# Kernel tuning notes

Hardware: AMD Instinct MI355X
Metric: run time of the kernel (lower is better)

The kernel has to match this reference:

```python
import jax, jax.numpy as jnp
import numpy as np

N_NODES = 100000
N_EDGES = 1600000
IN_DIM = 128
HID_DIM = 128
OUT_DIM = 2


def sage_conv(x, src, dst, deg_inv, W_l, W_r, b):
    # mean-aggregate neighbor features: messages flow src -> dst
    agg = jax.ops.segment_sum(x[src], dst, num_segments=N_NODES)  # [N, d_in]
    agg = agg * deg_inv[:, None]
    # PyG SAGEConv: out = lin_l(aggr) + lin_r(x); bias only on lin_l
    return agg @ W_l + x @ W_r + b


def setup_inputs() -> dict:
    key = jax.random.key(0)
    ks = jax.random.split(key, 9)
    x = jax.random.normal(ks[0], (N_NODES, IN_DIM), dtype=jnp.float32)
    edge_index = jax.random.randint(ks[1], (2, N_EDGES), 0, N_NODES, dtype=jnp.int64)

    def glorot(k, shape):
        lim = float(np.sqrt(6.0 / (shape[0] + shape[1])))
        return jax.random.uniform(k, shape, jnp.float32, -lim, lim)

    return {
        "x": x,
        "edge_index": edge_index,
        "W1_l": glorot(ks[2], (IN_DIM, HID_DIM)),
        "W1_r": glorot(ks[3], (IN_DIM, HID_DIM)),
        "b1": jnp.zeros((HID_DIM,), jnp.float32),
        "W2_l": glorot(ks[4], (HID_DIM, HID_DIM)),
        "W2_r": glorot(ks[5], (HID_DIM, HID_DIM)),
        "b2": jnp.zeros((HID_DIM,), jnp.float32),
        "W3_l": glorot(ks[6], (HID_DIM, OUT_DIM)),
        "W3_r": glorot(ks[7], (HID_DIM, OUT_DIM)),
        "b3": jnp.zeros((OUT_DIM,), jnp.float32),
    }


def reference(x, edge_index, W1_l, W1_r, b1, W2_l, W2_r, b2, W3_l, W3_r, b3):
    src, dst = edge_index[0], edge_index[1]
    # mean-aggregation normalization: 1/in-degree (clamped to >=1)
    deg = jax.ops.segment_sum(jnp.ones((N_EDGES,), jnp.float32), dst, num_segments=N_NODES)
    deg_inv = 1.0 / jnp.maximum(deg, 1.0)

    h = sage_conv(x, src, dst, deg_inv, W1_l, W1_r, b1)
    h = jax.nn.relu(h)  # dropout is identity in eval mode
    h = sage_conv(h, src, dst, deg_inv, W2_l, W2_r, b2)
    h = jax.nn.relu(h)
    h = sage_conv(h, src, dst, deg_inv, W3_l, W3_r, b3)
    h = jax.nn.relu(h)
    return jax.nn.log_softmax(h, axis=1)
```

## Files before the change

kernel.cpp:

```cpp
#include <hip/hip_runtime.h>
#include <hip/hip_bf16.h>
#include <math.h>

#define DIM 128

typedef __attribute__((ext_vector_type(8))) short bf16x8;
typedef __attribute__((ext_vector_type(4))) float f32x4;

__device__ __forceinline__ ushort f2bf(float f) {
  unsigned u = __float_as_uint(f);
  return (ushort)((u + 0x7FFFu + ((u >> 16) & 1u)) >> 16);
}
__device__ __forceinline__ float bf2f(ushort h) {
  return __uint_as_float(((unsigned)h) << 16);
}

__global__ __launch_bounds__(256) void prep_kernel(
    const int* __restrict__ dst, unsigned* __restrict__ deg, unsigned* __restrict__ rank, int E,
    const float* __restrict__ x, ushort* __restrict__ xh, long total,
    const float* __restrict__ W1l, const float* __restrict__ W1r,
    const float* __restrict__ W2l, const float* __restrict__ W2r,
    ushort* __restrict__ tabs, int H, int C) {
  int bid = blockIdx.x;
  if (bid < H) {
    int gid = bid * 256 + threadIdx.x;
    if (gid < E) rank[gid] = atomicAdd(&deg[dst[gid]], 1u);
    return;
  }
  bid -= H;
  if (bid < C) {
    long i = ((long)bid * 256 + threadIdx.x) * 4;
    if (i >= total) return;
    float4 v = *(const float4*)(x + i);
    uint2 Hh;
    Hh.x = (unsigned)f2bf(v.x) | ((unsigned)f2bf(v.y) << 16);
    Hh.y = (unsigned)f2bf(v.z) | ((unsigned)f2bf(v.w) << 16);
    *(uint2*)(xh + i) = Hh;
    return;
  }
  bid -= C;
  int m = bid >> 6;
  const float* W = (m == 0) ? W1l : (m == 1) ? W1r : (m == 2) ? W2l : W2r;
  ushort* Ht = tabs + (size_t)m * 32768;
  ushort* Lt = Ht + 16384;
  int idx = (bid & 63) * 256 + threadIdx.x;
  int k = idx >> 7, n = idx & 127;
  float v = W[idx];
  ushort h = f2bf(v);
  Ht[n * DIM + k] = h;
  Lt[n * DIM + k] = f2bf(v - bf2f(h));
}

__global__ __launch_bounds__(256) void scan_block_kernel(const unsigned* __restrict__ deg,
                                                         unsigned* __restrict__ excl,
                                                         unsigned* __restrict__ partial,
                                                         float* __restrict__ dinv, int N) {
  __shared__ unsigned s[256];
  int i = blockIdx.x * 256 + threadIdx.x;
  unsigned v = (i < N) ? deg[i] : 0u;
  if (i < N) dinv[i] = 1.0f / fmaxf((float)v, 1.0f);
  s[threadIdx.x] = v;
  __syncthreads();
#pragma unroll
  for (int d = 1; d < 256; d <<= 1) {
    unsigned t = (threadIdx.x >= d) ? s[threadIdx.x - d] : 0u;
    __syncthreads();
    s[threadIdx.x] += t;
    __syncthreads();
  }
  if (i < N) excl[i] = s[threadIdx.x] - v;
  if (threadIdx.x == 255) partial[blockIdx.x] = s[255];
}

__global__ __launch_bounds__(256) void scan_partials_kernel(unsigned* __restrict__ partial, int B) {
  __shared__ unsigned s[256];
  __shared__ unsigned carry;
  if (threadIdx.x == 0) carry = 0u;
  __syncthreads();
  for (int base = 0; base < B; base += 256) {
    int i = base + threadIdx.x;
    unsigned v = (i < B) ? partial[i] : 0u;
    s[threadIdx.x] = v;
    __syncthreads();
#pragma unroll
    for (int d = 1; d < 256; d <<= 1) {
      unsigned t = (threadIdx.x >= d) ? s[threadIdx.x - d] : 0u;
      __syncthreads();
      s[threadIdx.x] += t;
      __syncthreads();
    }
    if (i < B) partial[i] = carry + s[threadIdx.x] - v;
    __syncthreads();
    if (threadIdx.x == 0) carry += s[255];
    __syncthreads();
  }
}

__global__ __launch_bounds__(256) void add_offsets_kernel(const unsigned* __restrict__ excl,
                                                          const unsigned* __restrict__ partial,
                                                          unsigned* __restrict__ off, int N, int E) {
  int i = blockIdx.x * 256 + threadIdx.x;
  if (i < N) off[i] = excl[i] + partial[i >> 8];
  if (i == N) off[N] = (unsigned)E;
}

__global__ __launch_bounds__(256) void csr_fill_kernel(const int* __restrict__ src,
                                                       const int* __restrict__ dst,
                                                       const unsigned* __restrict__ rank,
                                                       const unsigned* __restrict__ off,
                                                       int* __restrict__ csr_src, int E) {
  int e = blockIdx.x * 256 + threadIdx.x;
  if (e >= E) return;
  csr_src[off[dst[e]] + rank[e]] = src[e];
}

__global__ __launch_bounds__(256) void gather_wave_kernel(
    const ushort* __restrict__ featH, const int* __restrict__ csr_src,
    const unsigned* __restrict__ off, const float* __restrict__ dinv,
    ushort* __restrict__ aggH, int N) {
  const int node = (blockIdx.x * 256 + threadIdx.x) >> 6;
  if (node >= N) return;
  const int lane = threadIdx.x & 63;
  const int eslot = lane >> 4;
  const int col = lane & 15;
  const unsigned beg = off[node], end = off[node + 1];
  const ushort* fbase = featH + col * 8;

  float acc[8];
#pragma unroll
  for (int t = 0; t < 8; ++t) acc[t] = 0.f;

  auto accum = [&](int4 v) {
    unsigned w0 = (unsigned)v.x, w1 = (unsigned)v.y, w2 = (unsigned)v.z, w3 = (unsigned)v.w;
    acc[0] += __uint_as_float(w0 << 16);
    acc[1] += __uint_as_float(w0 & 0xFFFF0000u);
    acc[2] += __uint_as_float(w1 << 16);
    acc[3] += __uint_as_float(w1 & 0xFFFF0000u);
    acc[4] += __uint_as_float(w2 << 16);
    acc[5] += __uint_as_float(w2 & 0xFFFF0000u);
    acc[6] += __uint_as_float(w3 << 16);
    acc[7] += __uint_as_float(w3 & 0xFFFF0000u);
  };

  unsigned base = beg;
  for (; base + 8 <= end; base += 8) {
    int s0 = csr_src[base + eslot];
    int s1 = csr_src[base + 4 + eslot];
    int4 v0 = *(const int4*)(fbase + (size_t)s0 * DIM);
    int4 v1 = *(const int4*)(fbase + (size_t)s1 * DIM);
    accum(v0);
    accum(v1);
  }
  for (unsigned e = base + eslot; e < end; e += 4) {
    int s = csr_src[e];
    int4 v = *(const int4*)(fbase + (size_t)s * DIM);
    accum(v);
  }

#pragma unroll
  for (int t = 0; t < 8; ++t) {
    acc[t] += __shfl_xor(acc[t], 32, 64);
    acc[t] += __shfl_xor(acc[t], 16, 64);
  }

  if (eslot == 0) {
    float di = dinv[node];
    unsigned ph[4];
#pragma unroll
    for (int t = 0; t < 4; ++t) {
      ph[t] = (unsigned)f2bf(acc[2 * t] * di) | ((unsigned)f2bf(acc[2 * t + 1] * di) << 16);
    }
    *(int4*)(aggH + (size_t)node * DIM + col * 8) =
        make_int4((int)ph[0], (int)ph[1], (int)ph[2], (int)ph[3]);
  }
}

__global__ __launch_bounds__(256) void sage_mfma_kernel(
    const ushort* __restrict__ aggH, const ushort* xH,
    const ushort* __restrict__ WlH, const ushort* __restrict__ WlL,
    const ushort* __restrict__ WrH, const ushort* __restrict__ WrL,
    const float* __restrict__ bias,
    const float* __restrict__ W3l, const float* __restrict__ W3r,
    ushort* outH, float* __restrict__ y, int N) {
  __shared__ ushort As[128 * 64];
  __shared__ ushort Bs[128 * 64];
  __shared__ float Wc[128][4];
  __shared__ float Yp[128][4][2];

  const int tid = threadIdx.x;
  const int bm = blockIdx.x * 128;
  const int wave = tid >> 6;
  const int lane = tid & 63;
  const int l15 = lane & 15;
  const int quad = lane >> 4;
  const int wm = wave >> 1;
  const int wn = wave & 1;

  if (W3l && tid < 128) {
    Wc[tid][0] = W3l[tid * 2 + 0];
    Wc[tid][1] = W3l[tid * 2 + 1];
    Wc[tid][2] = W3r[tid * 2 + 0];
    Wc[tid][3] = W3r[tid * 2 + 1];
  }

  f32x4 acc[4][4];
#pragma unroll
  for (int i = 0; i < 4; ++i)
#pragma unroll
    for (int j = 0; j < 4; ++j) acc[i][j] = (f32x4){0.f, 0.f, 0.f, 0.f};

  for (int it = 0; it < 8; ++it) {
    const int seg = it >> 1;
    const int kt = (it & 1) << 6;
    const ushort *Ap, *Wp;
    if (seg == 0)      { Ap = aggH; Wp = WlH; }
    else if (seg == 1) { Ap = aggH; Wp = WlL; }
    else if (seg == 2) { Ap = xH;   Wp = WrH; }
    else               { Ap = xH;   Wp = WrL; }
    __syncthreads();
#pragma unroll
    for (int c = 0; c < 4; ++c) {
      int flat = c * 256 + tid;
      int row = flat >> 3;
      int kg = flat & 7;
      int swz = (kg ^ (row & 7)) << 3;
      int grow = bm + row;
      if (grow >= N) grow = N - 1;
      *(int4*)(&As[row * 64 + swz]) = *(const int4*)(Ap + (size_t)grow * DIM + kt + kg * 8);
      *(int4*)(&Bs[row * 64 + swz]) = *(const int4*)(Wp + (size_t)row * DIM + kt + kg * 8);
    }
    __syncthreads();
#pragma unroll
    for (int ks = 0; ks < 2; ++ks) {
      bf16x8 af[4], bfr[4];
      int kg = (ks << 2) + quad;
#pragma unroll
      for (int i = 0; i < 4; ++i) {
        int ar = (wm << 6) + (i << 4) + l15;
        af[i] = *(const bf16x8*)(&As[ar * 64 + ((kg ^ (ar & 7)) << 3)]);
        int br = (wn << 6) + (i << 4) + l15;
        bfr[i] = *(const bf16x8*)(&Bs[br * 64 + ((kg ^ (br & 7)) << 3)]);
      }
#pragma unroll
      for (int i = 0; i < 4; ++i)
#pragma unroll
        for (int j = 0; j < 4; ++j)
          acc[i][j] = __builtin_amdgcn_mfma_f32_16x16x32_bf16(af[i], bfr[j], acc[i][j], 0, 0, 0);
    }
  }

  float bv[4];
#pragma unroll
  for (int j = 0; j < 4; ++j) bv[j] = bias[(wn << 6) + (j << 4) + l15];

#pragma unroll
  for (int i = 0; i < 4; ++i) {
#pragma unroll
    for (int r = 0; r < 4; ++r) {
      const int rowl = (wm << 6) + (i << 4) + (quad << 2) + r;
      const int grow = bm + rowl;
      float p0 = 0.f, p1 = 0.f, p2 = 0.f, p3 = 0.f;
#pragma unroll
      for (int j = 0; j < 4; ++j) {
        float v = fmaxf(acc[i][j][r] + bv[j], 0.f);
        ushort h = f2bf(v);
        if (grow < N) outH[(size_t)grow * DIM + (wn << 6) + (j << 4) + l15] = h;
        if (W3l) {
          float q = bf2f(h);
          int col = (wn << 6) + (j << 4) + l15;
          p0 += q * Wc[col][0];
          p1 += q * Wc[col][1];
          p2 += q * Wc[col][2];
          p3 += q * Wc[col][3];
        }
      }
      if (W3l) {
#pragma unroll
        for (int o = 1; o < 16; o <<= 1) {
          p0 += __shfl_xor(p0, o, 64);
          p1 += __shfl_xor(p1, o, 64);
          p2 += __shfl_xor(p2, o, 64);
          p3 += __shfl_xor(p3, o, 64);
        }
        if (l15 == 0) {
          Yp[rowl][0][wn] = p0;
          Yp[rowl][1][wn] = p1;
          Yp[rowl][2][wn] = p2;
          Yp[rowl][3][wn] = p3;
        }
      }
    }
  }

  if (W3l) {
    __syncthreads();
    for (int t = tid; t < 512; t += 256) {
      int row = t >> 2, c = t & 3;
      int grow = bm + row;
      if (grow < N) y[(size_t)grow * 4 + c] = Yp[row][c][0] + Yp[row][c][1];
    }
  }
}

__global__ __launch_bounds__(256) void final3_kernel(const float* __restrict__ y,
                                                     const int* __restrict__ csr_src,
                                                     const unsigned* __restrict__ off,
                                                     const float* __restrict__ dinv,
                                                     const float* __restrict__ b3,
                                                     float* __restrict__ out, int N) {
  int n = blockIdx.x * 256 + threadIdx.x;
  if (n >= N) return;
  unsigned beg = off[n], end = off[n + 1];
  float s0 = 0.f, s1 = 0.f;
  for (unsigned e = beg; e < end; ++e) {
    int s = csr_src[e];
    float2 v = *reinterpret_cast<const float2*>(&y[(size_t)s * 4]);
    s0 += v.x; s1 += v.y;
  }
  float di = dinv[n];
  float o0 = fmaxf(s0 * di + y[(size_t)n * 4 + 2] + b3[0], 0.f);
  float o1 = fmaxf(s1 * di + y[(size_t)n * 4 + 3] + b3[1], 0.f);
  float m = fmaxf(o0, o1);
  float l = m + logf(expf(o0 - m) + expf(o1 - m));
  out[n * 2 + 0] = o0 - l;
  out[n * 2 + 1] = o1 - l;
}

extern "C" void kernel_launch(void* const* d_in, const int* in_sizes, int n_in,
                              void* d_out, int out_size, void* d_ws, size_t ws_size,
                              hipStream_t stream) {
  const float* x   = (const float*)d_in[0];
  const int*   ei  = (const int*)d_in[1];
  const float* W1l = (const float*)d_in[2];
  const float* W1r = (const float*)d_in[3];
  const float* b1  = (const float*)d_in[4];
  const float* W2l = (const float*)d_in[5];
  const float* W2r = (const float*)d_in[6];
  const float* b2  = (const float*)d_in[7];
  const float* W3l = (const float*)d_in[8];
  const float* W3r = (const float*)d_in[9];
  const float* b3  = (const float*)d_in[10];

  const int N = in_sizes[0] / DIM;
  const int E = in_sizes[1] / 2;
  const int* src = ei;
  const int* dst = ei + E;
  const int B = (N + 255) / 256;

  char* ws = (char*)d_ws;
  size_t off_b = 0;
  auto alloc = [&](size_t bytes) {
    void* p = ws + off_b;
    off_b = (off_b + bytes + 255) & ~(size_t)255;
    return p;
  };
  unsigned* deg     = (unsigned*)alloc((size_t)N * 4);
  unsigned* excl    = (unsigned*)alloc((size_t)N * 4);
  unsigned* partial = (unsigned*)alloc((size_t)B * 4);
  unsigned* offs    = (unsigned*)alloc((size_t)(N + 1) * 4);
  unsigned* rank    = (unsigned*)alloc((size_t)E * 4);
  int*      csr_src = (int*)alloc((size_t)E * 4);
  float*    dinv    = (float*)alloc((size_t)N * 4);
  ushort*   xH      = (ushort*)alloc((size_t)N * DIM * 2);
  ushort*   aggH    = (ushort*)alloc((size_t)N * DIM * 2);
  ushort*   wtabs   = (ushort*)alloc((size_t)8 * 16384 * 2);
  float*    y       = (float*)alloc((size_t)N * 4 * 4);

  const int H = (E + 255) / 256;
  const int C = (int)(((size_t)N * DIM / 4 + 255) / 256);
  hipMemsetAsync(deg, 0, (size_t)N * 4, stream);
  prep_kernel<<<H + C + 256, 256, 0, stream>>>(dst, deg, rank, E, x, xH, (long)N * DIM,
                                               W1l, W1r, W2l, W2r, wtabs, H, C);

  scan_block_kernel<<<B, 256, 0, stream>>>(deg, excl, partial, dinv, N);
  scan_partials_kernel<<<1, 256, 0, stream>>>(partial, B);
  add_offsets_kernel<<<(N + 256) / 256, 256, 0, stream>>>(excl, partial, offs, N, E);
  csr_fill_kernel<<<(E + 255) / 256, 256, 0, stream>>>(src, dst, rank, offs, csr_src, E);

  const ushort* W1lH = wtabs;           const ushort* W1lL = wtabs + 16384;
  const ushort* W1rH = wtabs + 32768;   const ushort* W1rL = wtabs + 49152;
  const ushort* W2lH = wtabs + 65536;   const ushort* W2lL = wtabs + 81920;
  const ushort* W2rH = wtabs + 98304;   const ushort* W2rL = wtabs + 114688;

  const int gemm_grid = (N + 127) / 128;
  const int gather_grid = (N + 3) / 4;

  gather_wave_kernel<<<gather_grid, 256, 0, stream>>>(xH, csr_src, offs, dinv, aggH, N);
  sage_mfma_kernel<<<gemm_grid, 256, 0, stream>>>(aggH, xH, W1lH, W1lL, W1rH, W1rL, b1,
                                                  nullptr, nullptr, xH, nullptr, N);
  gather_wave_kernel<<<gather_grid, 256, 0, stream>>>(xH, csr_src, offs, dinv, aggH, N);
  sage_mfma_kernel<<<gemm_grid, 256, 0, stream>>>(aggH, xH, W2lH, W2lL, W2rH, W2rL, b2,
                                                  W3l, W3r, xH, y, N);
  final3_kernel<<<(N + 255) / 256, 256, 0, stream>>>(y, csr_src, offs, dinv, b3, (float*)d_out, N);
}
```

Before: 422.9 us.

## Interleave prep work, unroll gather by 4, and fuse hi/lo weight MFMA passes

The prep kernel now interleaves degree-atomic blocks with conversion and weight-split blocks in a 1:2 pattern, so atomic-bound and bandwidth-bound work run at the same time. The gather loop gains a 16-edge unrolled stage that keeps four outstanding row loads per lane. The GEMM loads the high and low bf16 weight tables together and issues both MFMAs per A-fragment, halving the A-tile reloads and barrier rounds. The extra B buffer raises LDS use, with the epilogue scratch moved into As, which may reduce occupancy.

```diff
diff --git a/kernel.cpp b/kernel.cpp
--- a/kernel.cpp
+++ b/kernel.cpp
@@ -21,15 +21,19 @@
     const float* __restrict__ W1l, const float* __restrict__ W1r,
     const float* __restrict__ W2l, const float* __restrict__ W2r,
     ushort* __restrict__ tabs, int H, int C) {
-  int bid = blockIdx.x;
-  if (bid < H) {
-    int gid = bid * 256 + threadIdx.x;
-    if (gid < E) rank[gid] = atomicAdd(&deg[dst[gid]], 1u);
+  const int bid = blockIdx.x;
+  const int r = bid % 3;
+  const int q = bid / 3;
+  if (r == 0) {
+    if (q < H) {
+      int gid = q * 256 + threadIdx.x;
+      if (gid < E) rank[gid] = atomicAdd(&deg[dst[gid]], 1u);
+    }
     return;
   }
-  bid -= H;
-  if (bid < C) {
-    long i = ((long)bid * 256 + threadIdx.x) * 4;
+  int id2 = q * 2 + (r - 1);
+  if (id2 < C) {
+    long i = ((long)id2 * 256 + threadIdx.x) * 4;
     if (i >= total) return;
     float4 v = *(const float4*)(x + i);
     uint2 Hh;
@@ -38,12 +42,13 @@
     *(uint2*)(xh + i) = Hh;
     return;
   }
-  bid -= C;
-  int m = bid >> 6;
+  id2 -= C;
+  if (id2 >= 256) return;
+  int m = id2 >> 6;
   const float* W = (m == 0) ? W1l : (m == 1) ? W1r : (m == 2) ? W2l : W2r;
   ushort* Ht = tabs + (size_t)m * 32768;
   ushort* Lt = Ht + 16384;
-  int idx = (bid & 63) * 256 + threadIdx.x;
+  int idx = (id2 & 63) * 256 + threadIdx.x;
   int k = idx >> 7, n = idx & 127;
   float v = W[idx];
   ushort h = f2bf(v);
@@ -143,13 +148,23 @@
   };
 
   unsigned base = beg;
+  for (; base + 16 <= end; base += 16) {
+    int s0 = csr_src[base + eslot];
+    int s1 = csr_src[base + 4 + eslot];
+    int s2 = csr_src[base + 8 + eslot];
+    int s3 = csr_src[base + 12 + eslot];
+    int4 v0 = *(const int4*)(fbase + (size_t)s0 * DIM);
+    int4 v1 = *(const int4*)(fbase + (size_t)s1 * DIM);
+    int4 v2 = *(const int4*)(fbase + (size_t)s2 * DIM);
+    int4 v3 = *(const int4*)(fbase + (size_t)s3 * DIM);
+    accum(v0); accum(v1); accum(v2); accum(v3);
+  }
   for (; base + 8 <= end; base += 8) {
     int s0 = csr_src[base + eslot];
     int s1 = csr_src[base + 4 + eslot];
     int4 v0 = *(const int4*)(fbase + (size_t)s0 * DIM);
     int4 v1 = *(const int4*)(fbase + (size_t)s1 * DIM);
-    accum(v0);
-    accum(v1);
+    accum(v0); accum(v1);
   }
   for (unsigned e = base + eslot; e < end; e += 4) {
     int s = csr_src[e];
@@ -183,9 +198,7 @@
     const float* __restrict__ W3l, const float* __restrict__ W3r,
     ushort* outH, float* __restrict__ y, int N) {
   __shared__ ushort As[128 * 64];
-  __shared__ ushort Bs[128 * 64];
-  __shared__ float Wc[128][4];
-  __shared__ float Yp[128][4][2];
+  __shared__ ushort Bs[2 * 128 * 64];
 
   const int tid = threadIdx.x;
   const int bm = blockIdx.x * 128;
@@ -196,27 +209,17 @@
   const int wm = wave >> 1;
   const int wn = wave & 1;
 
-  if (W3l && tid < 128) {
-    Wc[tid][0] = W3l[tid * 2 + 0];
-    Wc[tid][1] = W3l[tid * 2 + 1];
-    Wc[tid][2] = W3r[tid * 2 + 0];
-    Wc[tid][3] = W3r[tid * 2 + 1];
-  }
-
   f32x4 acc[4][4];
 #pragma unroll
   for (int i = 0; i < 4; ++i)
 #pragma unroll
     for (int j = 0; j < 4; ++j) acc[i][j] = (f32x4){0.f, 0.f, 0.f, 0.f};
 
-  for (int it = 0; it < 8; ++it) {
-    const int seg = it >> 1;
-    const int kt = (it & 1) << 6;
-    const ushort *Ap, *Wp;
-    if (seg == 0)      { Ap = aggH; Wp = WlH; }
-    else if (seg == 1) { Ap = aggH; Wp = WlL; }
-    else if (seg == 2) { Ap = xH;   Wp = WrH; }
-    else               { Ap = xH;   Wp = WrL; }
+  for (int g = 0; g < 4; ++g) {
+    const ushort* Ap = (g < 2) ? aggH : xH;
+    const ushort* WH = (g < 2) ? WlH : WrH;
+    const ushort* WL = (g < 2) ? WlL : WrL;
+    const int kt = (g & 1) << 6;
     __syncthreads();
 #pragma unroll
     for (int c = 0; c < 4; ++c) {
@@ -227,26 +230,52 @@
       int grow = bm + row;
       if (grow >= N) grow = N - 1;
       *(int4*)(&As[row * 64 + swz]) = *(const int4*)(Ap + (size_t)grow * DIM + kt + kg * 8);
-      *(int4*)(&Bs[row * 64 + swz]) = *(const int4*)(Wp + (size_t)row * DIM + kt + kg * 8);
+    }
+#pragma unroll
+    for (int c = 0; c < 8; ++c) {
+      int flat = c * 256 + tid;
+      int tbl = flat >> 10;
+      int row = (flat >> 3) & 127;
+      int kg = flat & 7;
+      int swz = (kg ^ (row & 7)) << 3;
+      const ushort* Wp = tbl ? WL : WH;
+      *(int4*)(&Bs[tbl * 8192 + row * 64 + swz]) =
+          *(const int4*)(Wp + (size_t)row * DIM + kt + kg * 8);
     }
     __syncthreads();
 #pragma unroll
     for (int ks = 0; ks < 2; ++ks) {
-      bf16x8 af[4], bfr[4];
+      bf16x8 af[4], bh[4], bl[4];
       int kg = (ks << 2) + quad;
 #pragma unroll
       for (int i = 0; i < 4; ++i) {
         int ar = (wm << 6) + (i << 4) + l15;
         af[i] = *(const bf16x8*)(&As[ar * 64 + ((kg ^ (ar & 7)) << 3)]);
         int br = (wn << 6) + (i << 4) + l15;
-        bfr[i] = *(const bf16x8*)(&Bs[br * 64 + ((kg ^ (br & 7)) << 3)]);
+        int bo = br * 64 + ((kg ^ (br & 7)) << 3);
+        bh[i] = *(const bf16x8*)(&Bs[bo]);
+        bl[i] = *(const bf16x8*)(&Bs[8192 + bo]);
       }
 #pragma unroll
       for (int i = 0; i < 4; ++i)
 #pragma unroll
-        for (int j = 0; j < 4; ++j)
-          acc[i][j] = __builtin_amdgcn_mfma_f32_16x16x32_bf16(af[i], bfr[j], acc[i][j], 0, 0, 0);
-    }
+        for (int j = 0; j < 4; ++j) {
+          acc[i][j] = __builtin_amdgcn_mfma_f32_16x16x32_bf16(af[i], bh[j], acc[i][j], 0, 0, 0);
+          acc[i][j] = __builtin_amdgcn_mfma_f32_16x16x32_bf16(af[i], bl[j], acc[i][j], 0, 0, 0);
+        }
+    }
+  }
+
+  __syncthreads();
+  float* WcF = reinterpret_cast<float*>(As);
+  float* YpF = reinterpret_cast<float*>(As) + 512;
+
+  if (W3l) {
+    for (int t = tid; t < 512; t += 256) {
+      int col = t >> 2, c = t & 3;
+      WcF[t] = (c < 2) ? W3l[col * 2 + c] : W3r[col * 2 + (c - 2)];
+    }
+    __syncthreads();
   }
 
   float bv[4];
@@ -266,12 +295,12 @@
         ushort h = f2bf(v);
         if (grow < N) outH[(size_t)grow * DIM + (wn << 6) + (j << 4) + l15] = h;
         if (W3l) {
-          float q = bf2f(h);
+          float qv = bf2f(h);
           int col = (wn << 6) + (j << 4) + l15;
-          p0 += q * Wc[col][0];
-          p1 += q * Wc[col][1];
-          p2 += q * Wc[col][2];
-          p3 += q * Wc[col][3];
+          p0 += qv * WcF[col * 4 + 0];
+          p1 += qv * WcF[col * 4 + 1];
+          p2 += qv * WcF[col * 4 + 2];
+          p3 += qv * WcF[col * 4 + 3];
         }
       }
       if (W3l) {
@@ -283,10 +312,10 @@
           p3 += __shfl_xor(p3, o, 64);
         }
         if (l15 == 0) {
-          Yp[rowl][0][wn] = p0;
-          Yp[rowl][1][wn] = p1;
-          Yp[rowl][2][wn] = p2;
-          Yp[rowl][3][wn] = p3;
+          YpF[(rowl * 4 + 0) * 2 + wn] = p0;
+          YpF[(rowl * 4 + 1) * 2 + wn] = p1;
+          YpF[(rowl * 4 + 2) * 2 + wn] = p2;
+          YpF[(rowl * 4 + 3) * 2 + wn] = p3;
         }
       }
     }
@@ -295,9 +324,8 @@
   if (W3l) {
     __syncthreads();
     for (int t = tid; t < 512; t += 256) {
-      int row = t >> 2, c = t & 3;
-      int grow = bm + row;
-      if (grow < N) y[(size_t)grow * 4 + c] = Yp[row][c][0] + Yp[row][c][1];
+      int grow = bm + (t >> 2);
+      if (grow < N) y[(size_t)grow * 4 + (t & 3)] = YpF[t * 2 + 0] + YpF[t * 2 + 1];
     }
   }
 }
@@ -368,9 +396,10 @@
 
   const int H = (E + 255) / 256;
   const int C = (int)(((size_t)N * DIM / 4 + 255) / 256);
+  const int third = (H > (C + 257) / 2) ? H : (C + 257) / 2;
   hipMemsetAsync(deg, 0, (size_t)N * 4, stream);
-  prep_kernel<<<H + C + 256, 256, 0, stream>>>(dst, deg, rank, E, x, xH, (long)N * DIM,
-                                               W1l, W1r, W2l, W2r, wtabs, H, C);
+  prep_kernel<<<third * 3, 256, 0, stream>>>(dst, deg, rank, E, x, xH, (long)N * DIM,
+                                             W1l, W1r, W2l, W2r, wtabs, H, C);
 
   scan_block_kernel<<<B, 256, 0, stream>>>(deg, excl, partial, dinv, N);
   scan_partials_kernel<<<1, 256, 0, stream>>>(partial, B);
```

After: 406.9 us. -3.8%, faster.
